# Kernel optimization log

Measured on AMD Instinct MI355X. Metric: run time of the kernel, lower is better.

The kernel has to match this reference:

```python
import jax, jax.numpy as jnp
import numpy as np

K = 16            # neighbors
RATIO = 0.25      # sampling ratio
BN_EPS = 1e-5


def setup_inputs() -> dict:
    key = jax.random.key(0)
    k1, k2, k3 = jax.random.split(key, 3)
    B, N, Cin, Cout = 8, 8192, 64, 128
    x = jax.random.normal(k1, (B, N, Cin), dtype=jnp.float32)
    p1 = jax.random.uniform(k2, (B, N, 3), dtype=jnp.float32)
    W = jax.random.normal(k3, (Cout, Cin), dtype=jnp.float32) * 0.05  # Conv1d(k=1, bias=False)
    gamma = jnp.ones((Cout,), dtype=jnp.float32)   # BatchNorm1d weight
    beta = jnp.zeros((Cout,), dtype=jnp.float32)   # BatchNorm1d bias
    return {"x": x, "p1": p1, "W": W, "gamma": gamma, "beta": beta}


def furthest_point_sample(p, M):
    """Greedy FPS. p: (B,N,3) -> (B,M) int32 indices. Starts at index 0 (CUDA impl convention)."""
    B, N, _ = p.shape
    first = jnp.zeros((B,), dtype=jnp.int32)
    mind = jnp.full((B, N), 1e10, dtype=p.dtype)

    def step(carry, _):
        mind, last = carry
        lp = jnp.take_along_axis(p, last[:, None, None].astype(jnp.int32), axis=1)  # (B,1,3)
        d = jnp.sum((p - lp) ** 2, axis=-1)          # (B,N)
        mind = jnp.minimum(mind, d)
        nxt = jnp.argmax(mind, axis=1).astype(jnp.int32)
        return (mind, nxt), nxt

    (_, _), rest = jax.lax.scan(step, (mind, first), None, length=M - 1)  # rest: (M-1,B)
    idx = jnp.concatenate([first[None, :], rest], axis=0)  # (M,B)
    return idx.T  # (B,M)


def reference(x, p1, W, gamma, beta):
    B, N, Cin = x.shape
    M = int(N * RATIO)

    # --- FPS sampling + gather coords ---
    fps_idx = furthest_point_sample(p1, M)                      # (B,M)
    p2 = jnp.take_along_axis(p1, fps_idx[:, :, None], axis=1)   # (B,M,3)

    # --- brute-force kNN of p1 around each p2 query ---
    d2 = (jnp.sum(p2 ** 2, -1)[:, :, None]
          - 2.0 * jnp.einsum('bmd,bnd->bmn', p2, p1)
          + jnp.sum(p1 ** 2, -1)[:, None, :])                   # (B,M,N)
    _, nbr = jax.lax.top_k(-d2, K)                              # (B,M,K) indices into N

    # --- shared MLP: 1x1 conv (no bias) + BatchNorm1d (training-mode stats) + ReLU ---
    h = jnp.einsum('bnc,oc->bno', x, W)                         # (B,N,Cout)
    mean = jnp.mean(h, axis=(0, 1))
    var = jnp.var(h, axis=(0, 1))
    h = (h - mean) * jax.lax.rsqrt(var + BN_EPS) * gamma + beta
    h = jax.nn.relu(h)

    # --- gather k neighbors per sampled point, max-pool over neighborhood ---
    feats = h[jnp.arange(B)[:, None, None], nbr]                # (B,M,K,Cout)
    y = jnp.max(feats, axis=2)                                  # (B,M,Cout)
    return y, p2
```

## Files before the change

### kernel.cpp

```cpp
#include <hip/hip_runtime.h>
#include <stdint.h>

#define Bb   8
#define Nn   8192
#define CIN  64
#define COUT 128
#define Mm   2048
#define KNN  16
#define NTOT (Bb*Nn)
#define NCONS 248

typedef unsigned long long ull;
typedef float v2f __attribute__((ext_vector_type(2)));

#define MAGIC 0x55AA1234u


__device__ __forceinline__ v2f pk_add(v2f a, v2f b)
{ v2f d; asm("v_pk_add_f32 %0, %1, %2" : "=v"(d) : "v"(a), "v"(b)); return d; }
__device__ __forceinline__ v2f pk_mul(v2f a, v2f b)
{ v2f d; asm("v_pk_mul_f32 %0, %1, %2" : "=v"(d) : "v"(a), "v"(b)); return d; }

__device__ __forceinline__ float wave_max16(float x)
{
    int v = __float_as_int(x), t;
    t = __builtin_amdgcn_update_dpp(v, v, 0x111, 0xf, 0xf, false);
    v = __float_as_int(fmaxf(__int_as_float(v), __int_as_float(t)));
    t = __builtin_amdgcn_update_dpp(v, v, 0x112, 0xf, 0xf, false);
    v = __float_as_int(fmaxf(__int_as_float(v), __int_as_float(t)));
    t = __builtin_amdgcn_update_dpp(v, v, 0x114, 0xf, 0xf, false);
    v = __float_as_int(fmaxf(__int_as_float(v), __int_as_float(t)));
    t = __builtin_amdgcn_update_dpp(v, v, 0x118, 0xf, 0xf, false);
    v = __float_as_int(fmaxf(__int_as_float(v), __int_as_float(t)));
    unsigned r0 = (unsigned)__builtin_amdgcn_readlane(v, 15);
    unsigned r1 = (unsigned)__builtin_amdgcn_readlane(v, 31);
    unsigned r2 = (unsigned)__builtin_amdgcn_readlane(v, 47);
    unsigned r3 = (unsigned)__builtin_amdgcn_readlane(v, 63);
    unsigned m0 = r0 > r1 ? r0 : r1;
    unsigned m1 = r2 > r3 ? r2 : r3;
    unsigned mm = m0 > m1 ? m0 : m1;
    return __uint_as_float(mm);
}

__device__ __forceinline__ ull d2key(
    float qx, float qy, float qz, float qn, float x, float y, float z, int j)
{
    float dot = __fadd_rn(__fadd_rn(__fmul_rn(qx, x), __fmul_rn(qy, y)),
                          __fmul_rn(qz, z));
    float cn  = __fadd_rn(__fadd_rn(__fmul_rn(x, x), __fmul_rn(y, y)),
                          __fmul_rn(z, z));
    float d2  = __fadd_rn(__fsub_rn(qn, __fadd_rn(dot, dot)), cn);
    unsigned int bits = __float_as_uint(d2);
    unsigned int u = bits ^ (((unsigned int)((int)bits >> 31)) | 0x80000000u);
    return ((ull)u << 32) | (unsigned int)j;
}

__global__ __launch_bounds__(512, 1)
void mega_kernel(const float* __restrict__ p1, float* __restrict__ p2out,
                 const float* __restrict__ x, const float* __restrict__ W,
                 const float* __restrict__ gamma, const float* __restrict__ beta,
                 float* __restrict__ h, float* __restrict__ stats,
                 unsigned int* done, ull* idxpub, float* __restrict__ y)
{
    __shared__ float px[Nn], py[Nn], pz[Nn];
    __shared__ alignas(16) ull wkey[2][8];
    const int tid = threadIdx.x;
    const int w = tid >> 6, lane = tid & 63;

    if (blockIdx.x < 8) {
        const int b = blockIdx.x;
        const float* pb = p1 + b * Nn * 3;

        for (int i = tid; i < Nn * 3; i += 512) {
            float v = pb[i];
            int pt = i / 3;
            int c  = i - pt * 3;
            if (c == 0) px[pt] = v; else if (c == 1) py[pt] = v; else pz[pt] = v;
        }
        __syncthreads();

        v2f ppx[8], ppy[8], ppz[8], mind[8];
#pragma unroll
        for (int i = 0; i < 8; ++i) {
            int j0 = tid * 16 + 2 * i;
            ppx[i] = (v2f){px[j0], px[j0 + 1]};
            ppy[i] = (v2f){py[j0], py[j0 + 1]};
            ppz[i] = (v2f){pz[j0], pz[j0 + 1]};
            mind[i] = (v2f){1e10f, 1e10f};
        }

        float lx = px[0], ly = py[0], lz = pz[0];
        if (tid == 0) {
            __hip_atomic_store(&idxpub[b * Mm], ((ull)MAGIC << 32) | 0ull,
                               __ATOMIC_RELAXED, __HIP_MEMORY_SCOPE_AGENT);
            int o = (b * Mm) * 3;
            p2out[o] = lx; p2out[o + 1] = ly; p2out[o + 2] = lz;
        }

        for (int m = 1; m < Mm; ++m) {
            const int buf = m & 1;
            float nx = -lx, ny = -ly, nz = -lz;
            v2f nx2 = (v2f){nx, nx}, ny2 = (v2f){ny, ny}, nz2 = (v2f){nz, nz};
            float bv0 = -1.0f, bv1 = -1.0f; int bj0 = 0, bj1 = 1;
#pragma unroll
            for (int i = 0; i < 8; ++i) {
                v2f dx = pk_add(ppx[i], nx2);
                v2f dy = pk_add(ppy[i], ny2);
                v2f dz = pk_add(ppz[i], nz2);
                v2f s  = pk_add(pk_add(pk_mul(dx, dx), pk_mul(dy, dy)),
                                pk_mul(dz, dz));
                float m0 = fminf(mind[i].x, s.x);
                float m1 = fminf(mind[i].y, s.y);
                mind[i].x = m0; mind[i].y = m1;
                if (m0 > bv0) { bv0 = m0; bj0 = 2 * i; }
                if (m1 > bv1) { bv1 = m1; bj1 = 2 * i + 1; }
            }
            float bestv; int bestj;
            if (bv1 > bv0 || (bv1 == bv0 && bj1 < bj0)) { bestv = bv1; bestj = bj1; }
            else                                        { bestv = bv0; bestj = bj0; }
            bestj += tid * 16;

            float wv = wave_max16(bestv);
            ull tie = __ballot(bestv == wv);
            int low = __ffsll((long long)tie) - 1;
            if (lane == low) {
                wkey[buf][w] = ((ull)__float_as_uint(wv) << 32) |
                               (unsigned int)(~(unsigned int)bestj);
            }
            __syncthreads();

            ull fk = wkey[buf][0];
#pragma unroll
            for (int q = 1; q < 8; ++q) { ull k = wkey[buf][q]; fk = k > fk ? k : fk; }
            int jw = (int)(~(unsigned int)fk);
            if (tid == 0) {
                __hip_atomic_store(&idxpub[b * Mm + m],
                                   ((ull)MAGIC << 32) | (ull)(unsigned)jw,
                                   __ATOMIC_RELAXED, __HIP_MEMORY_SCOPE_AGENT);
            }
            lx = px[jw]; ly = py[jw]; lz = pz[jw];
            if (tid == 0) {
                int o = (b * Mm + m) * 3;
                p2out[o] = lx; p2out[o + 1] = ly; p2out[o + 2] = lz;
            }
        }
        return;
    }

    const int cb = blockIdx.x - 8;
    const int cp = lane;
    {
        const float4* w0 = (const float4*)(W + (cp * 2) * CIN);
        const float4* w1 = (const float4*)(W + (cp * 2 + 1) * CIN);
        float s0 = 0.f, s1 = 0.f, q0 = 0.f, q1 = 0.f;
        for (int r0 = cb * 32 + w * 4; r0 < NTOT; r0 += NCONS * 32) {
            const float4* xp = (const float4*)(x + r0 * CIN);
            float a[4][2];
#pragma unroll
            for (int r = 0; r < 4; ++r) { a[r][0] = 0.f; a[r][1] = 0.f; }
#pragma unroll
            for (int k = 0; k < CIN / 4; ++k) {
                float4 wa = w0[k], wb = w1[k];
#pragma unroll
                for (int r = 0; r < 4; ++r) {
                    float4 xv = xp[r * 16 + k];
                    a[r][0] = fmaf(xv.x, wa.x, fmaf(xv.y, wa.y, fmaf(xv.z, wa.z, fmaf(xv.w, wa.w, a[r][0]))));
                    a[r][1] = fmaf(xv.x, wb.x, fmaf(xv.y, wb.y, fmaf(xv.z, wb.z, fmaf(xv.w, wb.w, a[r][1]))));
                }
            }
#pragma unroll
            for (int r = 0; r < 4; ++r) {
                *(float2*)(h + (r0 + r) * COUT + cp * 2) = make_float2(a[r][0], a[r][1]);
                s0 += a[r][0]; s1 += a[r][1];
                q0 = fmaf(a[r][0], a[r][0], q0); q1 = fmaf(a[r][1], a[r][1], q1);
            }
        }
        float4* comb = (float4*)px;
        comb[w * 64 + cp] = make_float4(s0, s1, q0, q1);
        __syncthreads();
        if (tid < 64) {
            float4 t = comb[cp];
#pragma unroll
            for (int j = 1; j < 8; ++j) {
                float4 o = comb[j * 64 + cp];
                t.x += o.x; t.y += o.y; t.z += o.z; t.w += o.w;
            }
            atomicAdd(&stats[2 * cp], t.x);     atomicAdd(&stats[2 * cp + 1], t.y);
            atomicAdd(&stats[128 + 2 * cp], t.z); atomicAdd(&stats[128 + 2 * cp + 1], t.w);
        }
        __syncthreads();
        if (tid == 0) {
            __hip_atomic_fetch_add(done, 1u, __ATOMIC_RELEASE,
                                   __HIP_MEMORY_SCOPE_AGENT);
            while (__hip_atomic_load(done, __ATOMIC_ACQUIRE,
                                     __HIP_MEMORY_SCOPE_AGENT) < NCONS)
                __builtin_amdgcn_s_sleep(2);
        }
        __syncthreads();
    }

    float sc0, sc1, bi0, bi1;
    {
        float mean0 = stats[2 * cp] * (1.0f / 65536.0f);
        float mean1 = stats[2 * cp + 1] * (1.0f / 65536.0f);
        float var0  = stats[128 + 2 * cp] * (1.0f / 65536.0f) - mean0 * mean0;
        float var1  = stats[128 + 2 * cp + 1] * (1.0f / 65536.0f) - mean1 * mean1;
        sc0 = gamma[2 * cp] / sqrtf(var0 + 1e-5f);
        sc1 = gamma[2 * cp + 1] / sqrtf(var1 + 1e-5f);
        bi0 = beta[2 * cp] - mean0 * sc0;
        bi1 = beta[2 * cp + 1] - mean1 * sc1;
    }

    const int b = cb / 31;
    const int k = cb - b * 31;
    const float* pb = p1 + b * Nn * 3;

    for (int i = tid; i < Nn * 3; i += 512) {
        float v = pb[i];
        int pt = i / 3;
        int c  = i - pt * 3;
        if (c == 0) px[pt] = v; else if (c == 1) py[pt] = v; else pz[pt] = v;
    }
    __syncthreads();

    const int c0 = lane * 2;
    const ull INV = ~0ull;

    for (int t = w; k + 31 * t < Mm; t += 8) {
        const int m = k + 31 * t;
        const int qrow = b * Mm + m;

        ull pv;
        for (;;) {
            pv = __hip_atomic_load(&idxpub[qrow], __ATOMIC_RELAXED,
                                   __HIP_MEMORY_SCOPE_AGENT);
            if ((unsigned)(pv >> 32) == MAGIC) break;
            __builtin_amdgcn_s_sleep(2);
        }
        const int jq = (int)(pv & 0x1FFFull);
        const float qx = px[jq], qy = py[jq], qz = pz[jq];
        const float qn = __fadd_rn(__fadd_rn(__fmul_rn(qx, qx), __fmul_rn(qy, qy)),
                                   __fmul_rn(qz, qz));

        ull k1 = INV, k2 = INV, k3 = INV;
#pragma unroll 4
        for (int i = 0; i < 128; ++i) {
            int j = lane + (i << 6);
            ull key = d2key(qx, qy, qz, qn, px[j], py[j], pz[j], j);
            bool b1 = key < k1, b2 = key < k2, b3 = key < k3;
            ull n1 = b1 ? key : k1;
            ull n2 = b1 ? k1 : (b2 ? key : k2);
            ull n3 = b2 ? k2 : (b3 ? key : k3);
            k1 = n1; k2 = n2; k3 = n3;
        }

        float a0 = -1e30f, a1 = -1e30f;
        for (int r = 0; r < KNN; ++r) {
            ull wk = k1;
#pragma unroll
            for (int off = 1; off < 64; off <<= 1) {
                ull ok = __shfl_xor(wk, off, 64);
                wk = ok < wk ? ok : wk;
            }
            const int n = (int)(unsigned int)(wk & 0xFFFFFFFFull);
            const float2 v = *(const float2*)(h + (((b << 13) + n) * COUT) + c0);
            if (k1 == wk) { k1 = k2; k2 = k3; k3 = INV; }
            if (k1 == INV) {
                for (int i = 0; i < 128; ++i) {
                    int j = lane + (i << 6);
                    ull key = d2key(qx, qy, qz, qn, px[j], py[j], pz[j], j);
                    if (key > wk) {
                        bool b1 = key < k1, b2 = key < k2, b3 = key < k3;
                        ull n1 = b1 ? key : k1;
                        ull n2 = b1 ? k1 : (b2 ? key : k2);
                        ull n3 = b2 ? k2 : (b3 ? key : k3);
                        k1 = n1; k2 = n2; k3 = n3;
                    }
                }
            }
            a0 = fmaxf(a0, fmaf(v.x, sc0, bi0));
            a1 = fmaxf(a1, fmaf(v.y, sc1, bi1));
        }
        a0 = fmaxf(a0, 0.0f); a1 = fmaxf(a1, 0.0f);
        *(float2*)(y + qrow * COUT + c0) = make_float2(a0, a1);
    }
}

extern "C" void kernel_launch(void* const* d_in, const int* in_sizes, int n_in,
                              void* d_out, int out_size, void* d_ws, size_t ws_size,
                              hipStream_t stream)
{
    const float* x     = (const float*)d_in[0];
    const float* p1    = (const float*)d_in[1];
    const float* W     = (const float*)d_in[2];
    const float* gamma = (const float*)d_in[3];
    const float* beta  = (const float*)d_in[4];

    float* y  = (float*)d_out;
    float* p2 = (float*)d_out + Bb * Mm * COUT;

    char*  ws     = (char*)d_ws;
    float* h      = (float*)ws;
    ull*   idxpub = (ull*)(ws + 33619968);
    float* stats  = (float*)(ws + 35717120);
    unsigned int* done = (unsigned int*)(ws + 35718144);

    hipMemsetAsync(stats, 0, 2048, stream);
    mega_kernel<<<256, 512, 0, stream>>>(p1, p2, x, W, gamma, beta,
                                         h, stats, done, idxpub, y);
}
```

Before: 2.072 ms.

## Halve block size and carry winner coordinates through FPS reduction

Blocks shrink from 512 to 256 threads, so each FPS thread now holds 32 points and the cross-wave reduction only has 4 wave keys to combine. Each wave also publishes its candidate's coordinates next to its key, which removes the dependent LDS lookup of the winning point after the barrier. A raw s_barrier replaces __syncthreads. Writing p2 moves from the serial FPS loop to the kNN consumer blocks. The trade-off is that consumer blocks now have half as many waves for the GEMM/BN and kNN phases, and FPS threads carry more registers.

```diff
diff --git a/kernel.cpp b/kernel.cpp
--- a/kernel.cpp
+++ b/kernel.cpp
@@ -55,7 +55,7 @@
     return ((ull)u << 32) | (unsigned int)j;
 }
 
-__global__ __launch_bounds__(512, 1)
+__global__ __launch_bounds__(256, 1)
 void mega_kernel(const float* __restrict__ p1, float* __restrict__ p2out,
                  const float* __restrict__ x, const float* __restrict__ W,
                  const float* __restrict__ gamma, const float* __restrict__ beta,
@@ -63,7 +63,8 @@
                  unsigned int* done, ull* idxpub, float* __restrict__ y)
 {
     __shared__ float px[Nn], py[Nn], pz[Nn];
-    __shared__ alignas(16) ull wkey[2][8];
+    __shared__ ull    skey[2][4];
+    __shared__ float4 scoord[2][4];
     const int tid = threadIdx.x;
     const int w = tid >> 6, lane = tid & 63;
 
@@ -71,7 +72,7 @@
         const int b = blockIdx.x;
         const float* pb = p1 + b * Nn * 3;
 
-        for (int i = tid; i < Nn * 3; i += 512) {
+        for (int i = tid; i < Nn * 3; i += 256) {
             float v = pb[i];
             int pt = i / 3;
             int c  = i - pt * 3;
@@ -79,10 +80,10 @@
         }
         __syncthreads();
 
-        v2f ppx[8], ppy[8], ppz[8], mind[8];
-#pragma unroll
-        for (int i = 0; i < 8; ++i) {
-            int j0 = tid * 16 + 2 * i;
+        v2f ppx[16], ppy[16], ppz[16], mind[16];
+#pragma unroll
+        for (int i = 0; i < 16; ++i) {
+            int j0 = tid * 32 + 2 * i;
             ppx[i] = (v2f){px[j0], px[j0 + 1]};
             ppy[i] = (v2f){py[j0], py[j0 + 1]};
             ppz[i] = (v2f){pz[j0], pz[j0 + 1]};
@@ -93,8 +94,6 @@
         if (tid == 0) {
             __hip_atomic_store(&idxpub[b * Mm], ((ull)MAGIC << 32) | 0ull,
                                __ATOMIC_RELAXED, __HIP_MEMORY_SCOPE_AGENT);
-            int o = (b * Mm) * 3;
-            p2out[o] = lx; p2out[o + 1] = ly; p2out[o + 2] = lz;
         }
 
         for (int m = 1; m < Mm; ++m) {
@@ -103,7 +102,7 @@
             v2f nx2 = (v2f){nx, nx}, ny2 = (v2f){ny, ny}, nz2 = (v2f){nz, nz};
             float bv0 = -1.0f, bv1 = -1.0f; int bj0 = 0, bj1 = 1;
 #pragma unroll
-            for (int i = 0; i < 8; ++i) {
+            for (int i = 0; i < 16; ++i) {
                 v2f dx = pk_add(ppx[i], nx2);
                 v2f dy = pk_add(ppy[i], ny2);
                 v2f dz = pk_add(ppz[i], nz2);
@@ -118,30 +117,38 @@
             float bestv; int bestj;
             if (bv1 > bv0 || (bv1 == bv0 && bj1 < bj0)) { bestv = bv1; bestj = bj1; }
             else                                        { bestv = bv0; bestj = bj0; }
-            bestj += tid * 16;
+            bestj += tid * 32;
+
+            float sx = px[bestj], sy = py[bestj], sz = pz[bestj];
 
             float wv = wave_max16(bestv);
             ull tie = __ballot(bestv == wv);
             int low = __ffsll((long long)tie) - 1;
             if (lane == low) {
-                wkey[buf][w] = ((ull)__float_as_uint(wv) << 32) |
+                skey[buf][w] = ((ull)__float_as_uint(wv) << 32) |
                                (unsigned int)(~(unsigned int)bestj);
-            }
-            __syncthreads();
-
-            ull fk = wkey[buf][0];
-#pragma unroll
-            for (int q = 1; q < 8; ++q) { ull k = wkey[buf][q]; fk = k > fk ? k : fk; }
+                scoord[buf][w] = make_float4(sx, sy, sz, 0.0f);
+            }
+            asm volatile("s_waitcnt lgkmcnt(0)\n\ts_barrier" ::: "memory");
+
+            ull k0 = skey[buf][0], k1 = skey[buf][1];
+            ull k2 = skey[buf][2], k3 = skey[buf][3];
+            float4 q0 = scoord[buf][0], q1 = scoord[buf][1];
+            float4 q2 = scoord[buf][2], q3 = scoord[buf][3];
+            bool s1 = k1 > k0;
+            ull ka = s1 ? k1 : k0;
+            float ax = s1 ? q1.x : q0.x, ay = s1 ? q1.y : q0.y, az = s1 ? q1.z : q0.z;
+            bool s2 = k3 > k2;
+            ull kb = s2 ? k3 : k2;
+            float bx = s2 ? q3.x : q2.x, by = s2 ? q3.y : q2.y, bz = s2 ? q3.z : q2.z;
+            bool s3 = kb > ka;
+            ull fk = s3 ? kb : ka;
+            lx = s3 ? bx : ax; ly = s3 ? by : ay; lz = s3 ? bz : az;
             int jw = (int)(~(unsigned int)fk);
             if (tid == 0) {
                 __hip_atomic_store(&idxpub[b * Mm + m],
                                    ((ull)MAGIC << 32) | (ull)(unsigned)jw,
                                    __ATOMIC_RELAXED, __HIP_MEMORY_SCOPE_AGENT);
-            }
-            lx = px[jw]; ly = py[jw]; lz = pz[jw];
-            if (tid == 0) {
-                int o = (b * Mm + m) * 3;
-                p2out[o] = lx; p2out[o + 1] = ly; p2out[o + 2] = lz;
             }
         }
         return;
@@ -153,7 +160,7 @@
         const float4* w0 = (const float4*)(W + (cp * 2) * CIN);
         const float4* w1 = (const float4*)(W + (cp * 2 + 1) * CIN);
         float s0 = 0.f, s1 = 0.f, q0 = 0.f, q1 = 0.f;
-        for (int r0 = cb * 32 + w * 4; r0 < NTOT; r0 += NCONS * 32) {
+        for (int r0 = cb * 16 + w * 4; r0 < NTOT; r0 += NCONS * 16) {
             const float4* xp = (const float4*)(x + r0 * CIN);
             float a[4][2];
 #pragma unroll
@@ -181,11 +188,11 @@
         if (tid < 64) {
             float4 t = comb[cp];
 #pragma unroll
-            for (int j = 1; j < 8; ++j) {
+            for (int j = 1; j < 4; ++j) {
                 float4 o = comb[j * 64 + cp];
                 t.x += o.x; t.y += o.y; t.z += o.z; t.w += o.w;
             }
-            atomicAdd(&stats[2 * cp], t.x);     atomicAdd(&stats[2 * cp + 1], t.y);
+            atomicAdd(&stats[2 * cp], t.x);       atomicAdd(&stats[2 * cp + 1], t.y);
             atomicAdd(&stats[128 + 2 * cp], t.z); atomicAdd(&stats[128 + 2 * cp + 1], t.w);
         }
         __syncthreads();
@@ -215,7 +222,7 @@
     const int k = cb - b * 31;
     const float* pb = p1 + b * Nn * 3;
 
-    for (int i = tid; i < Nn * 3; i += 512) {
+    for (int i = tid; i < Nn * 3; i += 256) {
         float v = pb[i];
         int pt = i / 3;
         int c  = i - pt * 3;
@@ -226,7 +233,7 @@
     const int c0 = lane * 2;
     const ull INV = ~0ull;
 
-    for (int t = w; k + 31 * t < Mm; t += 8) {
+    for (int t = w; k + 31 * t < Mm; t += 4) {
         const int m = k + 31 * t;
         const int qrow = b * Mm + m;
 
@@ -239,6 +246,11 @@
         }
         const int jq = (int)(pv & 0x1FFFull);
         const float qx = px[jq], qy = py[jq], qz = pz[jq];
+        if (lane == 0) {
+            p2out[qrow * 3]     = qx;
+            p2out[qrow * 3 + 1] = qy;
+            p2out[qrow * 3 + 2] = qz;
+        }
         const float qn = __fadd_rn(__fadd_rn(__fmul_rn(qx, qx), __fmul_rn(qy, qy)),
                                    __fmul_rn(qz, qz));
 
@@ -306,6 +318,6 @@
     unsigned int* done = (unsigned int*)(ws + 35718144);
 
     hipMemsetAsync(stats, 0, 2048, stream);
-    mega_kernel<<<256, 512, 0, stream>>>(p1, p2, x, W, gamma, beta,
+    mega_kernel<<<256, 256, 0, stream>>>(p1, p2, x, W, gamma, beta,
                                          h, stats, done, idxpub, y);
 }
```

Result: no change. 2.046 ms (-1.2%).
